# Kernel tuning notes

Measured on AMD Instinct MI355X. Metric: run time of the kernel, lower is better.

The kernel has to match this reference:

```python
import jax, jax.numpy as jnp
import numpy as np

EPS = 1e-5
N, K, CIN, COUT = 100000, 27, 64, 128


def sparse_conv(x, nbr, W):
    # x: [N, C]; nbr: [N, K] with sentinel index N meaning 'no neighbor'
    x_pad = jnp.concatenate([x, jnp.zeros((1, x.shape[1]), x.dtype)], axis=0)  # [N+1, C]
    g = x_pad[nbr]  # gather: [N, K, C]
    return jnp.einsum('nkc,kcd->nd', g, W)  # per-offset GEMM, scatter to output sites


def bn_relu(y, gamma, beta):
    # BatchNorm over active sites (training-mode batch statistics), then ReLU
    mu = y.mean(axis=0)
    var = y.var(axis=0)
    return jax.nn.relu((y - mu) * jax.lax.rsqrt(var + EPS) * gamma + beta)


def setup_inputs() -> dict:
    key = jax.random.key(0)
    ks = jax.random.split(key, 5)
    x = jax.random.normal(ks[0], (N, CIN), dtype=jnp.float32)
    # sentinel N indicates missing neighbor (maps to zero-padded row)
    nbr = jax.random.randint(ks[1], (N, K), 0, N + 1)
    W1 = jax.random.normal(ks[2], (K, CIN, COUT), dtype=jnp.float32) * (1.0 / np.sqrt(K * CIN))
    W2 = jax.random.normal(ks[3], (K, COUT, COUT), dtype=jnp.float32) * (1.0 / np.sqrt(K * COUT))
    W_skip = jax.random.normal(ks[4], (CIN, COUT), dtype=jnp.float32) * (1.0 / np.sqrt(CIN))
    return {
        'x': x, 'nbr': nbr,
        'W1': W1, 'gamma1': jnp.ones((COUT,), jnp.float32), 'beta1': jnp.zeros((COUT,), jnp.float32),
        'W2': W2, 'gamma2': jnp.ones((COUT,), jnp.float32), 'beta2': jnp.zeros((COUT,), jnp.float32),
        'W_skip': W_skip,
    }


def reference(x, nbr, W1, gamma1, beta1, W2, gamma2, beta2, W_skip):
    identity = x @ W_skip                      # 1x1 conv skip (same coords)
    h = bn_relu(sparse_conv(x, nbr, W1), gamma1, beta1)
    h = bn_relu(sparse_conv(h, nbr, W2), gamma2, beta2)
    return h + identity
```

## Files before the change

### kernel.cpp

```cpp
#include <hip/hip_runtime.h>
#include <hip/hip_bf16.h>

#define NSITES 100000
#define KOFFS 27
#define CIN 64
#define COUT 128

typedef unsigned short u16;
typedef __attribute__((ext_vector_type(8))) short s16x8;
typedef __attribute__((ext_vector_type(4))) float f32x4;

static __device__ __forceinline__ u16 f2bf(float f) {
    union { float f; unsigned u; } x; x.f = f;
    return (u16)((x.u + 0x7FFFu + ((x.u >> 16) & 1u)) >> 16);
}
static __device__ __forceinline__ float bf2f(u16 v) {
    union { unsigned u; float f; } x; x.u = ((unsigned)v) << 16;
    return x.f;
}

static __device__ __forceinline__ void lds_barrier() {
    asm volatile("s_waitcnt lgkmcnt(0)" ::: "memory");
    __builtin_amdgcn_s_barrier();
    __builtin_amdgcn_sched_barrier(0);
}

__global__ void prep_kernel(const float* __restrict__ W1, const float* __restrict__ W2,
                            const float* __restrict__ Wsk,
                            u16* __restrict__ W1t, u16* __restrict__ W2t,
                            u16* __restrict__ Wskt, float* __restrict__ zero_area) {
    int i = blockIdx.x * 256 + threadIdx.x;
    if (i < 27 * 64 * 128) {
        int k = i / 8192, r = i & 8191, d = r >> 6, c = r & 63;
        W1t[i] = f2bf(W1[k * 8192 + c * 128 + d]);
        return;
    }
    i -= 27 * 64 * 128;
    if (i < 27 * 128 * 128) {
        int k = i / 16384, r = i & 16383, d = r >> 7, c = r & 127;
        W2t[i] = f2bf(W2[k * 16384 + c * 128 + d]);
        return;
    }
    i -= 27 * 128 * 128;
    if (i < 8192) {
        int d = i >> 6, c = i & 63;
        Wskt[i] = f2bf(Wsk[c * 128 + d]);
        return;
    }
    i -= 8192;
    zero_area[i] = 0.0f;
}

__global__ void convert_x_kernel(const float* __restrict__ x, u16* __restrict__ xb) {
    long long e = ((long long)blockIdx.x * 256 + threadIdx.x) * 8;
    if (e >= (long long)(NSITES + 1) * CIN) return;
    s16x8 o;
    if (e < (long long)NSITES * CIN) {
        float4 v0 = *(const float4*)(x + e);
        float4 v1 = *(const float4*)(x + e + 4);
        o[0] = (short)f2bf(v0.x); o[1] = (short)f2bf(v0.y);
        o[2] = (short)f2bf(v0.z); o[3] = (short)f2bf(v0.w);
        o[4] = (short)f2bf(v1.x); o[5] = (short)f2bf(v1.y);
        o[6] = (short)f2bf(v1.z); o[7] = (short)f2bf(v1.w);
    } else {
#pragma unroll
        for (int j = 0; j < 8; ++j) o[j] = 0;
    }
    *(s16x8*)(xb + e) = o;
}

template <int CK, bool IDENT_FUSE, bool STATS>
__global__ __launch_bounds__(256, 3) void conv_kernel(
    const u16* __restrict__ xin, const int* __restrict__ nbr,
    const u16* __restrict__ Wt, u16* __restrict__ yout,
    float* __restrict__ psum, float* __restrict__ psq, int nk_unused,
    const u16* __restrict__ Wskt, float* __restrict__ outid) {
    constexpr int STRIDE = CK + 4;
    constexpr int KSTEPS = CK / 32;
    constexpr int CPR = CK / 8;
    constexpr int RPP = 256 / CPR;
    constexpr int NPASS = 64 / RPP;
    __shared__ __align__(16) u16 a_tile[2][64 * STRIDE];
    __shared__ int nbr_tile[64 * KOFFS];

    const int tid = threadIdx.x;
    const int wave = tid >> 6;
    const int lane = tid & 63;
    const int m = lane & 15;
    const int q = lane >> 4;
    const int n0 = blockIdx.x * 64;
    const int wc = wave * 32;
    const int srow = tid / CPR;
    const int schunk = tid % CPR;

    for (int i = tid; i < 64 * KOFFS; i += 256) {
        int r = i / KOFFS;
        int kk = i - r * KOFFS;
        int row = n0 + r;
        nbr_tile[i] = (row < NSITES) ? nbr[row * KOFFS + kk] : NSITES;
    }
    __syncthreads();

    f32x4 acc[4][2];
#pragma unroll
    for (int rt = 0; rt < 4; ++rt)
#pragma unroll
        for (int ct = 0; ct < 2; ++ct)
#pragma unroll
            for (int r = 0; r < 4; ++r) acc[rt][ct][r] = 0.0f;

    s16x8 gA[NPASS], gB[NPASS];
    s16x8 bA[2][KSTEPS], bB[2][KSTEPS];

    auto gload = [&](s16x8 (&g)[NPASS], int kk) {
#pragma unroll
        for (int p = 0; p < NPASS; ++p) {
            int r = p * RPP + srow;
            g[p] = *(const s16x8*)(xin + (long long)nbr_tile[r * KOFFS + kk] * CK + schunk * 8);
        }
    };
    auto bload = [&](s16x8 (&b)[2][KSTEPS], int kk) {
        const u16* wb = Wt + (long long)kk * (COUT * CK);
#pragma unroll
        for (int ct = 0; ct < 2; ++ct)
#pragma unroll
            for (int ks = 0; ks < KSTEPS; ++ks)
                b[ct][ks] = *(const s16x8*)(wb + (wc + ct * 16 + m) * CK + ks * 32 + q * 8);
    };
    auto awrite = [&](s16x8 (&g)[NPASS], int buf) {
#pragma unroll
        for (int p = 0; p < NPASS; ++p)
            *(s16x8*)(&a_tile[buf][(p * RPP + srow) * STRIDE + schunk * 8]) = g[p];
    };
    auto mfma_from = [&](int buf, s16x8 (&b)[2][KSTEPS]) {
        __builtin_amdgcn_s_setprio(1);
#pragma unroll
        for (int ks = 0; ks < KSTEPS; ++ks) {
            s16x8 af[4];
#pragma unroll
            for (int rt = 0; rt < 4; ++rt)
                af[rt] = *(const s16x8*)(&a_tile[buf][(rt * 16 + m) * STRIDE + ks * 32 + q * 8]);
#pragma unroll
            for (int rt = 0; rt < 4; ++rt)
#pragma unroll
                for (int ct = 0; ct < 2; ++ct)
                    acc[rt][ct] = __builtin_amdgcn_mfma_f32_16x16x32_bf16(
                        af[rt], b[ct][ks], acc[rt][ct], 0, 0, 0);
        }
        __builtin_amdgcn_s_setprio(0);
    };

    gload(gA, 0);
    bload(bA, 0);
    awrite(gA, 0);
    gload(gA, 1);
    bload(bB, 1);
    gload(gB, 2);
    lds_barrier();

    auto conv_iter = [&](int k, s16x8 (&g)[NPASS], s16x8 (&bcur)[2][KSTEPS]) {
        awrite(g, (k + 1) & 1);
        gload(g, k + 3);
        lds_barrier();
        mfma_from(k & 1, bcur);
        bload(bcur, k + 2);
        lds_barrier();
    };

    for (int k = 0; k < 24; k += 2) {
        conv_iter(k, gA, bA);
        conv_iter(k + 1, gB, bB);
    }
    awrite(gA, 1);
    lds_barrier();
    mfma_from(0, bA);
    bload(bA, 26);
    lds_barrier();
    awrite(gB, 0);
    lds_barrier();
    mfma_from(1, bB);
    lds_barrier();
    mfma_from(0, bA);

#pragma unroll
    for (int rt = 0; rt < 4; ++rt) {
        int rowb = n0 + rt * 16 + q * 4;
#pragma unroll
        for (int ct = 0; ct < 2; ++ct) {
            int col = wc + ct * 16 + m;
#pragma unroll
            for (int r = 0; r < 4; ++r) {
                int row = rowb + r;
                if (row < NSITES) yout[(long long)row * COUT + col] = f2bf(acc[rt][ct][r]);
            }
        }
    }

    if (STATS) {
#pragma unroll
        for (int ct = 0; ct < 2; ++ct) {
            float s = 0.f, ss = 0.f;
#pragma unroll
            for (int rt = 0; rt < 4; ++rt)
#pragma unroll
                for (int r = 0; r < 4; ++r) {
                    float v = acc[rt][ct][r];
                    s += v; ss += v * v;
                }
            s += __shfl_xor(s, 16); ss += __shfl_xor(ss, 16);
            s += __shfl_xor(s, 32); ss += __shfl_xor(ss, 32);
            if (q == 0) {
                int col = wc + ct * 16 + m;
                int slot = blockIdx.x & 63;
                atomicAdd(psum + slot * COUT + col, s);
                atomicAdd(psq + slot * COUT + col, ss);
            }
        }
    }

    if (IDENT_FUSE) {
        lds_barrier();
#pragma unroll
        for (int rt = 0; rt < 4; ++rt)
#pragma unroll
            for (int ct = 0; ct < 2; ++ct)
#pragma unroll
                for (int r = 0; r < 4; ++r) acc[rt][ct][r] = 0.0f;
        s16x8 aid[NPASS];
#pragma unroll
        for (int p = 0; p < NPASS; ++p) {
            int row = n0 + p * RPP + srow;
            long long idx = (row < NSITES) ? row : NSITES;
            aid[p] = *(const s16x8*)(xin + idx * CK + schunk * 8);
        }
        s16x8 bfi[2][KSTEPS];
#pragma unroll
        for (int ct = 0; ct < 2; ++ct)
#pragma unroll
            for (int ks = 0; ks < KSTEPS; ++ks)
                bfi[ct][ks] = *(const s16x8*)(Wskt + (wc + ct * 16 + m) * CK + ks * 32 + q * 8);
        awrite(aid, 0);
        lds_barrier();
        mfma_from(0, bfi);
#pragma unroll
        for (int rt = 0; rt < 4; ++rt) {
            int rowb = n0 + rt * 16 + q * 4;
#pragma unroll
            for (int ct = 0; ct < 2; ++ct) {
                int col = wc + ct * 16 + m;
#pragma unroll
                for (int r = 0; r < 4; ++r) {
                    int row = rowb + r;
                    if (row < NSITES) outid[(long long)row * COUT + col] = acc[rt][ct][r];
                }
            }
        }
    }
}

__global__ void bn_stats_kernel(const float* __restrict__ psum, const float* __restrict__ psq,
                                const float* __restrict__ gamma, const float* __restrict__ beta,
                                float* __restrict__ ab) {
    int col = threadIdx.x;
    float s = 0.f, ss = 0.f;
    for (int i = 0; i < 64; ++i) { s += psum[i * COUT + col]; ss += psq[i * COUT + col]; }
    const float inv_n = 1.0f / (float)NSITES;
    float mu = s * inv_n;
    float var = ss * inv_n - mu * mu;
    float rs = rsqrtf(var + 1e-5f);
    float a = gamma[col] * rs;
    ab[col] = a;
    ab[COUT + col] = beta[col] - mu * a;
}

__global__ void bn_apply_kernel(const u16* __restrict__ y, const float* __restrict__ ab,
                                u16* __restrict__ h) {
    long long e = ((long long)blockIdx.x * 256 + threadIdx.x) * 8;
    if (e >= (long long)(NSITES + 1) * COUT) return;
    s16x8 o;
    if (e < (long long)NSITES * COUT) {
        int cb = (int)(e & (COUT - 1));
        s16x8 v = *(const s16x8*)(y + e);
#pragma unroll
        for (int j = 0; j < 8; ++j) {
            float r = bf2f((u16)v[j]) * ab[cb + j] + ab[COUT + cb + j];
            o[j] = (short)f2bf(fmaxf(r, 0.f));
        }
    } else {
#pragma unroll
        for (int j = 0; j < 8; ++j) o[j] = 0;
    }
    *(s16x8*)(h + e) = o;
}

__global__ void final_kernel(const u16* __restrict__ y, const float* __restrict__ ab,
                             float* __restrict__ out) {
    long long e = ((long long)blockIdx.x * 256 + threadIdx.x) * 8;
    if (e >= (long long)NSITES * COUT) return;
    int cb = (int)(e & (COUT - 1));
    s16x8 v = *(const s16x8*)(y + e);
    float4 i0 = *(const float4*)(out + e);
    float4 i1 = *(const float4*)(out + e + 4);
    float is[8] = {i0.x, i0.y, i0.z, i0.w, i1.x, i1.y, i1.z, i1.w};
    float os[8];
#pragma unroll
    for (int j = 0; j < 8; ++j) {
        float r = bf2f((u16)v[j]) * ab[cb + j] + ab[COUT + cb + j];
        os[j] = fmaxf(r, 0.f) + is[j];
    }
    *(float4*)(out + e) = make_float4(os[0], os[1], os[2], os[3]);
    *(float4*)(out + e + 4) = make_float4(os[4], os[5], os[6], os[7]);
}

extern "C" void kernel_launch(void* const* d_in, const int* in_sizes, int n_in,
                              void* d_out, int out_size, void* d_ws, size_t ws_size,
                              hipStream_t stream) {
    const float* x   = (const float*)d_in[0];
    const int*   nbr = (const int*)d_in[1];
    const float* W1  = (const float*)d_in[2];
    const float* g1  = (const float*)d_in[3];
    const float* b1  = (const float*)d_in[4];
    const float* W2  = (const float*)d_in[5];
    const float* g2  = (const float*)d_in[6];
    const float* b2  = (const float*)d_in[7];
    const float* Wsk = (const float*)d_in[8];
    float* out = (float*)d_out;

    char* ws = (char*)d_ws;
    u16*   xb   = (u16*)(ws);
    u16*   W1t  = (u16*)(ws + 12800128);
    u16*   W2t  = (u16*)(ws + 13242496);
    u16*   Wskt = (u16*)(ws + 14127232);
    u16*   y    = (u16*)(ws + 14143616);
    u16*   h1   = (u16*)(ws + 39743616);
    float* ps1  = (float*)(ws + 65343872);
    float* pq1  = ps1 + 8192;
    float* ps2  = pq1 + 8192;
    float* pq2  = ps2 + 8192;
    float* ab1  = pq2 + 8192;
    float* ab2  = ab1 + 256;

    const int NBLK = (NSITES + 63) / 64;

    prep_kernel<<<2752, 256, 0, stream>>>(W1, W2, Wsk, W1t, W2t, Wskt, ps1);
    convert_x_kernel<<<3126, 256, 0, stream>>>(x, xb);
    conv_kernel<64, true, true><<<NBLK, 256, 0, stream>>>(xb, nbr, W1t, y, ps1, pq1, KOFFS, Wskt, out);
    bn_stats_kernel<<<1, 128, 0, stream>>>(ps1, pq1, g1, b1, ab1);
    bn_apply_kernel<<<6251, 256, 0, stream>>>(y, ab1, h1);
    conv_kernel<128, false, true><<<NBLK, 256, 0, stream>>>(h1, nbr, W2t, y, ps2, pq2, KOFFS, nullptr, nullptr);
    bn_stats_kernel<<<1, 128, 0, stream>>>(ps2, pq2, g2, b2, ab2);
    final_kernel<<<6250, 256, 0, stream>>>(y, ab2, out);
}
```

Before: 446.3 us.

## Fuse BN1 apply and ReLU into second conv's gather, add nontemporal memory ops

Removes the separate bn_apply kernel. The second sparse conv now gathers the raw conv1 output and applies the BN affine transform plus ReLU per element before writing to LDS. Sentinel neighbors are redirected to row 0 and masked to zero, so no padded row is needed. This saves a full read and write of the 25 MB intermediate, but the normalization is recomputed for each of the 27 gathers, which adds VALU work to the conv's LDS-write path. Nontemporal loads and stores are also applied to nbr, the conv outputs and the final kernel.

```diff
diff --git a/kernel.cpp b/kernel.cpp
--- a/kernel.cpp
+++ b/kernel.cpp
@@ -69,12 +69,13 @@
     *(s16x8*)(xb + e) = o;
 }
 
-template <int CK, bool IDENT_FUSE, bool STATS>
+template <int CK, bool IDENT_FUSE, bool STATS, bool TRANSFORM>
 __global__ __launch_bounds__(256, 3) void conv_kernel(
     const u16* __restrict__ xin, const int* __restrict__ nbr,
     const u16* __restrict__ Wt, u16* __restrict__ yout,
     float* __restrict__ psum, float* __restrict__ psq, int nk_unused,
-    const u16* __restrict__ Wskt, float* __restrict__ outid) {
+    const u16* __restrict__ Wskt, float* __restrict__ outid,
+    const float* __restrict__ abst) {
     constexpr int STRIDE = CK + 4;
     constexpr int KSTEPS = CK / 32;
     constexpr int CPR = CK / 8;
@@ -93,11 +94,22 @@
     const int srow = tid / CPR;
     const int schunk = tid % CPR;
 
+    float a8[8], b8[8];
+    if constexpr (TRANSFORM) {
+        const int cb = schunk * 8;
+#pragma unroll
+        for (int j = 0; j < 8; ++j) {
+            a8[j] = abst[cb + j];
+            b8[j] = abst[COUT + cb + j];
+        }
+    }
+
     for (int i = tid; i < 64 * KOFFS; i += 256) {
         int r = i / KOFFS;
         int kk = i - r * KOFFS;
         int row = n0 + r;
-        nbr_tile[i] = (row < NSITES) ? nbr[row * KOFFS + kk] : NSITES;
+        nbr_tile[i] = (row < NSITES) ? __builtin_nontemporal_load(&nbr[row * KOFFS + kk])
+                                     : NSITES;
     }
     __syncthreads();
 
@@ -110,13 +122,22 @@
             for (int r = 0; r < 4; ++r) acc[rt][ct][r] = 0.0f;
 
     s16x8 gA[NPASS], gB[NPASS];
+    int   sA[NPASS], sB[NPASS];
     s16x8 bA[2][KSTEPS], bB[2][KSTEPS];
 
-    auto gload = [&](s16x8 (&g)[NPASS], int kk) {
+    auto gload = [&](s16x8 (&g)[NPASS], int (&sen)[NPASS], int kk) {
 #pragma unroll
         for (int p = 0; p < NPASS; ++p) {
             int r = p * RPP + srow;
-            g[p] = *(const s16x8*)(xin + (long long)nbr_tile[r * KOFFS + kk] * CK + schunk * 8);
+            int idx = nbr_tile[r * KOFFS + kk];
+            long long gi;
+            if constexpr (TRANSFORM) {
+                sen[p] = (idx == NSITES);
+                gi = sen[p] ? 0 : idx;
+            } else {
+                gi = idx;
+            }
+            g[p] = *(const s16x8*)(xin + gi * CK + schunk * 8);
         }
     };
     auto bload = [&](s16x8 (&b)[2][KSTEPS], int kk) {
@@ -127,10 +148,22 @@
             for (int ks = 0; ks < KSTEPS; ++ks)
                 b[ct][ks] = *(const s16x8*)(wb + (wc + ct * 16 + m) * CK + ks * 32 + q * 8);
     };
-    auto awrite = [&](s16x8 (&g)[NPASS], int buf) {
-#pragma unroll
-        for (int p = 0; p < NPASS; ++p)
-            *(s16x8*)(&a_tile[buf][(p * RPP + srow) * STRIDE + schunk * 8]) = g[p];
+    auto awrite = [&](s16x8 (&g)[NPASS], int (&sen)[NPASS], int buf) {
+#pragma unroll
+        for (int p = 0; p < NPASS; ++p) {
+            s16x8 o;
+            if constexpr (TRANSFORM) {
+#pragma unroll
+                for (int j = 0; j < 8; ++j) {
+                    float v = bf2f((u16)g[p][j]);
+                    v = fmaxf(v * a8[j] + b8[j], 0.f);
+                    o[j] = sen[p] ? (short)0 : (short)f2bf(v);
+                }
+            } else {
+                o = g[p];
+            }
+            *(s16x8*)(&a_tile[buf][(p * RPP + srow) * STRIDE + schunk * 8]) = o;
+        }
     };
     auto mfma_from = [&](int buf, s16x8 (&b)[2][KSTEPS]) {
         __builtin_amdgcn_s_setprio(1);
@@ -150,17 +183,18 @@
         __builtin_amdgcn_s_setprio(0);
     };
 
-    gload(gA, 0);
+    gload(gA, sA, 0);
     bload(bA, 0);
-    awrite(gA, 0);
-    gload(gA, 1);
+    awrite(gA, sA, 0);
+    gload(gA, sA, 1);
     bload(bB, 1);
-    gload(gB, 2);
-    lds_barrier();
-
-    auto conv_iter = [&](int k, s16x8 (&g)[NPASS], s16x8 (&bcur)[2][KSTEPS]) {
-        awrite(g, (k + 1) & 1);
-        gload(g, k + 3);
+    gload(gB, sB, 2);
+    lds_barrier();
+
+    auto conv_iter = [&](int k, s16x8 (&g)[NPASS], int (&sen)[NPASS],
+                         s16x8 (&bcur)[2][KSTEPS]) {
+        awrite(g, sen, (k + 1) & 1);
+        gload(g, sen, k + 3);
         lds_barrier();
         mfma_from(k & 1, bcur);
         bload(bcur, k + 2);
@@ -168,15 +202,15 @@
     };
 
     for (int k = 0; k < 24; k += 2) {
-        conv_iter(k, gA, bA);
-        conv_iter(k + 1, gB, bB);
-    }
-    awrite(gA, 1);
+        conv_iter(k, gA, sA, bA);
+        conv_iter(k + 1, gB, sB, bB);
+    }
+    awrite(gA, sA, 1);
     lds_barrier();
     mfma_from(0, bA);
     bload(bA, 26);
     lds_barrier();
-    awrite(gB, 0);
+    awrite(gB, sB, 0);
     lds_barrier();
     mfma_from(1, bB);
     lds_barrier();
@@ -191,7 +225,9 @@
 #pragma unroll
             for (int r = 0; r < 4; ++r) {
                 int row = rowb + r;
-                if (row < NSITES) yout[(long long)row * COUT + col] = f2bf(acc[rt][ct][r]);
+                if (row < NSITES)
+                    __builtin_nontemporal_store((short)f2bf(acc[rt][ct][r]),
+                                                (short*)yout + (long long)row * COUT + col);
             }
         }
     }
@@ -239,7 +275,10 @@
 #pragma unroll
             for (int ks = 0; ks < KSTEPS; ++ks)
                 bfi[ct][ks] = *(const s16x8*)(Wskt + (wc + ct * 16 + m) * CK + ks * 32 + q * 8);
-        awrite(aid, 0);
+        int sdum[NPASS];
+#pragma unroll
+        for (int p = 0; p < NPASS; ++p) sdum[p] = 0;
+        awrite(aid, sdum, 0);
         lds_barrier();
         mfma_from(0, bfi);
 #pragma unroll
@@ -251,7 +290,9 @@
 #pragma unroll
                 for (int r = 0; r < 4; ++r) {
                     int row = rowb + r;
-                    if (row < NSITES) outid[(long long)row * COUT + col] = acc[rt][ct][r];
+                    if (row < NSITES)
+                        __builtin_nontemporal_store(acc[rt][ct][r],
+                                                    outid + (long long)row * COUT + col);
                 }
             }
         }
@@ -273,43 +314,27 @@
     ab[COUT + col] = beta[col] - mu * a;
 }
 
-__global__ void bn_apply_kernel(const u16* __restrict__ y, const float* __restrict__ ab,
-                                u16* __restrict__ h) {
-    long long e = ((long long)blockIdx.x * 256 + threadIdx.x) * 8;
-    if (e >= (long long)(NSITES + 1) * COUT) return;
-    s16x8 o;
-    if (e < (long long)NSITES * COUT) {
-        int cb = (int)(e & (COUT - 1));
-        s16x8 v = *(const s16x8*)(y + e);
-#pragma unroll
-        for (int j = 0; j < 8; ++j) {
-            float r = bf2f((u16)v[j]) * ab[cb + j] + ab[COUT + cb + j];
-            o[j] = (short)f2bf(fmaxf(r, 0.f));
-        }
-    } else {
-#pragma unroll
-        for (int j = 0; j < 8; ++j) o[j] = 0;
-    }
-    *(s16x8*)(h + e) = o;
-}
-
 __global__ void final_kernel(const u16* __restrict__ y, const float* __restrict__ ab,
                              float* __restrict__ out) {
     long long e = ((long long)blockIdx.x * 256 + threadIdx.x) * 8;
     if (e >= (long long)NSITES * COUT) return;
     int cb = (int)(e & (COUT - 1));
-    s16x8 v = *(const s16x8*)(y + e);
-    float4 i0 = *(const float4*)(out + e);
-    float4 i1 = *(const float4*)(out + e + 4);
-    float is[8] = {i0.x, i0.y, i0.z, i0.w, i1.x, i1.y, i1.z, i1.w};
-    float os[8];
-#pragma unroll
-    for (int j = 0; j < 8; ++j) {
+    s16x8 v = __builtin_nontemporal_load((const s16x8*)(y + e));
+    f32x4 i0 = __builtin_nontemporal_load((const f32x4*)(out + e));
+    f32x4 i1 = __builtin_nontemporal_load((const f32x4*)(out + e + 4));
+    f32x4 o0, o1;
+#pragma unroll
+    for (int j = 0; j < 4; ++j) {
         float r = bf2f((u16)v[j]) * ab[cb + j] + ab[COUT + cb + j];
-        os[j] = fmaxf(r, 0.f) + is[j];
-    }
-    *(float4*)(out + e) = make_float4(os[0], os[1], os[2], os[3]);
-    *(float4*)(out + e + 4) = make_float4(os[4], os[5], os[6], os[7]);
+        o0[j] = fmaxf(r, 0.f) + i0[j];
+    }
+#pragma unroll
+    for (int j = 0; j < 4; ++j) {
+        float r = bf2f((u16)v[4 + j]) * ab[cb + 4 + j] + ab[COUT + cb + 4 + j];
+        o1[j] = fmaxf(r, 0.f) + i1[j];
+    }
+    __builtin_nontemporal_store(o0, (f32x4*)(out + e));
+    __builtin_nontemporal_store(o1, (f32x4*)(out + e + 4));
 }
 
 extern "C" void kernel_launch(void* const* d_in, const int* in_sizes, int n_in,
@@ -332,7 +357,7 @@
     u16*   W2t  = (u16*)(ws + 13242496);
     u16*   Wskt = (u16*)(ws + 14127232);
     u16*   y    = (u16*)(ws + 14143616);
-    u16*   h1   = (u16*)(ws + 39743616);
+    u16*   y2   = (u16*)(ws + 39743616);
     float* ps1  = (float*)(ws + 65343872);
     float* pq1  = ps1 + 8192;
     float* ps2  = pq1 + 8192;
@@ -344,10 +369,11 @@
 
     prep_kernel<<<2752, 256, 0, stream>>>(W1, W2, Wsk, W1t, W2t, Wskt, ps1);
     convert_x_kernel<<<3126, 256, 0, stream>>>(x, xb);
-    conv_kernel<64, true, true><<<NBLK, 256, 0, stream>>>(xb, nbr, W1t, y, ps1, pq1, KOFFS, Wskt, out);
+    conv_kernel<64, true, true, false><<<NBLK, 256, 0, stream>>>(
+        xb, nbr, W1t, y, ps1, pq1, KOFFS, Wskt, out, nullptr);
     bn_stats_kernel<<<1, 128, 0, stream>>>(ps1, pq1, g1, b1, ab1);
-    bn_apply_kernel<<<6251, 256, 0, stream>>>(y, ab1, h1);
-    conv_kernel<128, false, true><<<NBLK, 256, 0, stream>>>(h1, nbr, W2t, y, ps2, pq2, KOFFS, nullptr, nullptr);
+    conv_kernel<128, false, true, true><<<NBLK, 256, 0, stream>>>(
+        y, nbr, W2t, y2, ps2, pq2, KOFFS, nullptr, nullptr, ab1);
     bn_stats_kernel<<<1, 128, 0, stream>>>(ps2, pq2, g2, b2, ab2);
-    final_kernel<<<6250, 256, 0, stream>>>(y, ab2, out);
-}
+    final_kernel<<<6250, 256, 0, stream>>>(y2, ab2, out);
+}
```

Result: slower. 468.8 us (+5.0%).

## Store activations in channel-sliced layout and use 32x32x16 MFMA in sparse conv

Applied to the files above, without the earlier changes.

Activations (converted x and BN output h1) are now stored as 16-channel slices, [C/16][N+1][16], so each gather fetches one 32-byte slice per neighbor. The conv kernel iterates over (slice, group of 4 offsets) and stages four neighbor offsets per LDS buffer. The 16x16x32 MFMAs are replaced by 32x32x16 MFMAs with two f32x16 accumulators, and launch bounds rise to 4 blocks per CU. The aim is less LDS/register pressure and better occupancy, traded against smaller, more scattered gather transactions and more pipeline iterations.

```diff
diff --git a/kernel.cpp b/kernel.cpp
--- a/kernel.cpp
+++ b/kernel.cpp
@@ -5,10 +5,12 @@
 #define KOFFS 27
 #define CIN 64
 #define COUT 128
+#define NROWS1 (NSITES + 1)
 
 typedef unsigned short u16;
 typedef __attribute__((ext_vector_type(8))) short s16x8;
 typedef __attribute__((ext_vector_type(4))) float f32x4;
+typedef __attribute__((ext_vector_type(16))) float f32x16;
 
 static __device__ __forceinline__ u16 f2bf(float f) {
     union { float f; unsigned u; } x; x.f = f;
@@ -53,9 +55,11 @@
 
 __global__ void convert_x_kernel(const float* __restrict__ x, u16* __restrict__ xb) {
     long long e = ((long long)blockIdx.x * 256 + threadIdx.x) * 8;
-    if (e >= (long long)(NSITES + 1) * CIN) return;
+    if (e >= (long long)NROWS1 * CIN) return;
+    int row = (int)(e >> 6);
+    int col = (int)(e & 63);
     s16x8 o;
-    if (e < (long long)NSITES * CIN) {
+    if (row < NSITES) {
         float4 v0 = *(const float4*)(x + e);
         float4 v1 = *(const float4*)(x + e + 4);
         o[0] = (short)f2bf(v0.x); o[1] = (short)f2bf(v0.y);
@@ -66,32 +70,32 @@
 #pragma unroll
         for (int j = 0; j < 8; ++j) o[j] = 0;
     }
-    *(s16x8*)(xb + e) = o;
-}
-
-template <int CK, bool IDENT_FUSE, bool STATS>
-__global__ __launch_bounds__(256, 3) void conv_kernel(
+    *(s16x8*)(xb + ((size_t)(col >> 4) * NROWS1 + row) * 16 + (col & 15)) = o;
+}
+
+template <int NSL, bool IDENT_FUSE, bool STATS>
+__global__ __launch_bounds__(256, 4) void conv_kernel(
     const u16* __restrict__ xin, const int* __restrict__ nbr,
     const u16* __restrict__ Wt, u16* __restrict__ yout,
-    float* __restrict__ psum, float* __restrict__ psq, int nk_unused,
+    float* __restrict__ psum, float* __restrict__ psq,
     const u16* __restrict__ Wskt, float* __restrict__ outid) {
-    constexpr int STRIDE = CK + 4;
-    constexpr int KSTEPS = CK / 32;
-    constexpr int CPR = CK / 8;
-    constexpr int RPP = 256 / CPR;
-    constexpr int NPASS = 64 / RPP;
-    __shared__ __align__(16) u16 a_tile[2][64 * STRIDE];
+    constexpr int CK = NSL * 16;
+    constexpr int NIT = NSL * 7;
+    constexpr int USTRIDE = 24;
+    constexpr int UNIT = 64 * USTRIDE;
+    constexpr int BUF = 4 * UNIT;
+    __shared__ __align__(16) u16 a_tile[2 * BUF];
     __shared__ int nbr_tile[64 * KOFFS];
 
     const int tid = threadIdx.x;
     const int wave = tid >> 6;
     const int lane = tid & 63;
-    const int m = lane & 15;
-    const int q = lane >> 4;
+    const int l31 = lane & 31;
+    const int hi = lane >> 5;
     const int n0 = blockIdx.x * 64;
     const int wc = wave * 32;
-    const int srow = tid / CPR;
-    const int schunk = tid % CPR;
+    const int su = tid >> 6;
+    const int srow = tid & 63;
 
     for (int i = tid; i < 64 * KOFFS; i += 256) {
         int r = i / KOFFS;
@@ -101,159 +105,134 @@
     }
     __syncthreads();
 
-    f32x4 acc[4][2];
-#pragma unroll
-    for (int rt = 0; rt < 4; ++rt)
-#pragma unroll
-        for (int ct = 0; ct < 2; ++ct)
-#pragma unroll
-            for (int r = 0; r < 4; ++r) acc[rt][ct][r] = 0.0f;
-
-    s16x8 gA[NPASS], gB[NPASS];
-    s16x8 bA[2][KSTEPS], bB[2][KSTEPS];
-
-    auto gload = [&](s16x8 (&g)[NPASS], int kk) {
-#pragma unroll
-        for (int p = 0; p < NPASS; ++p) {
-            int r = p * RPP + srow;
-            g[p] = *(const s16x8*)(xin + (long long)nbr_tile[r * KOFFS + kk] * CK + schunk * 8);
+    f32x16 acc0, acc1;
+#pragma unroll
+    for (int j = 0; j < 16; ++j) { acc0[j] = 0.0f; acc1[j] = 0.0f; }
+
+    s16x8 gA[2], gB[2];
+    s16x8 bA[4], bB[4];
+
+    auto gload = [&](s16x8 (&g)[2], int dit) {
+        int grp = dit % 7, s = dit / 7;
+        int gsz = (grp == 6) ? 3 : 4;
+        if (su < gsz) {
+            int k = grp * 4 + su;
+            const u16* base = xin + ((size_t)s * NROWS1 +
+                                     (size_t)nbr_tile[srow * KOFFS + k]) * 16;
+            g[0] = *(const s16x8*)(base);
+            g[1] = *(const s16x8*)(base + 8);
         }
     };
-    auto bload = [&](s16x8 (&b)[2][KSTEPS], int kk) {
-        const u16* wb = Wt + (long long)kk * (COUT * CK);
-#pragma unroll
-        for (int ct = 0; ct < 2; ++ct)
-#pragma unroll
-            for (int ks = 0; ks < KSTEPS; ++ks)
-                b[ct][ks] = *(const s16x8*)(wb + (wc + ct * 16 + m) * CK + ks * 32 + q * 8);
+    auto bload = [&](s16x8 (&b)[4], int dit) {
+        int grp = dit % 7, s = dit / 7;
+        int gsz = (grp == 6) ? 3 : 4;
+        const u16* wb = Wt + (size_t)(wc + l31) * CK + s * 16 + hi * 8;
+#pragma unroll
+        for (int u = 0; u < 4; ++u)
+            if (u < gsz) b[u] = *(const s16x8*)(wb + (size_t)(grp * 4 + u) * COUT * CK);
     };
-    auto awrite = [&](s16x8 (&g)[NPASS], int buf) {
-#pragma unroll
-        for (int p = 0; p < NPASS; ++p)
-            *(s16x8*)(&a_tile[buf][(p * RPP + srow) * STRIDE + schunk * 8]) = g[p];
+    auto awrite = [&](s16x8 (&g)[2], int dit) {
+        int grp = dit % 7;
+        int gsz = (grp == 6) ? 3 : 4;
+        if (su < gsz) {
+            u16* d = a_tile + (dit & 1) * BUF + su * UNIT + srow * USTRIDE;
+            *(s16x8*)(d) = g[0];
+            *(s16x8*)(d + 8) = g[1];
+        }
     };
-    auto mfma_from = [&](int buf, s16x8 (&b)[2][KSTEPS]) {
+    auto domfma = [&](int it, s16x8 (&b)[4]) {
+        int grp = it % 7;
+        int gsz = (grp == 6) ? 3 : 4;
+        const u16* base = a_tile + (it & 1) * BUF + l31 * USTRIDE + hi * 8;
         __builtin_amdgcn_s_setprio(1);
 #pragma unroll
-        for (int ks = 0; ks < KSTEPS; ++ks) {
-            s16x8 af[4];
-#pragma unroll
-            for (int rt = 0; rt < 4; ++rt)
-                af[rt] = *(const s16x8*)(&a_tile[buf][(rt * 16 + m) * STRIDE + ks * 32 + q * 8]);
-#pragma unroll
-            for (int rt = 0; rt < 4; ++rt)
-#pragma unroll
-                for (int ct = 0; ct < 2; ++ct)
-                    acc[rt][ct] = __builtin_amdgcn_mfma_f32_16x16x32_bf16(
-                        af[rt], b[ct][ks], acc[rt][ct], 0, 0, 0);
+        for (int u = 0; u < 4; ++u) {
+            if (u < gsz) {
+                s16x8 a0 = *(const s16x8*)(base + u * UNIT);
+                s16x8 a1 = *(const s16x8*)(base + u * UNIT + 32 * USTRIDE);
+                acc0 = __builtin_amdgcn_mfma_f32_32x32x16_bf16(a0, b[u], acc0, 0, 0, 0);
+                acc1 = __builtin_amdgcn_mfma_f32_32x32x16_bf16(a1, b[u], acc1, 0, 0, 0);
+            }
         }
         __builtin_amdgcn_s_setprio(0);
     };
 
-    gload(gA, 0);
-    bload(bA, 0);
-    awrite(gA, 0);
-    gload(gA, 1);
-    bload(bB, 1);
-    gload(gB, 2);
+    gload(gA, 0); bload(bA, 0);
+    awrite(gA, 0); gload(gA, 1); bload(bB, 1); gload(gB, 2);
     lds_barrier();
 
-    auto conv_iter = [&](int k, s16x8 (&g)[NPASS], s16x8 (&bcur)[2][KSTEPS]) {
-        awrite(g, (k + 1) & 1);
-        gload(g, k + 3);
+    for (int it = 0; it + 4 < NIT; it += 2) {
+        awrite(gA, it + 1); gload(gA, it + 3); lds_barrier();
+        domfma(it, bA); bload(bA, it + 2); lds_barrier();
+        awrite(gB, it + 2); gload(gB, it + 4); lds_barrier();
+        domfma(it + 1, bB); bload(bB, it + 3); lds_barrier();
+    }
+    awrite(gA, NIT - 3); gload(gA, NIT - 1); lds_barrier();
+    domfma(NIT - 4, bA); bload(bA, NIT - 2); lds_barrier();
+    awrite(gB, NIT - 2); lds_barrier();
+    domfma(NIT - 3, bB); bload(bB, NIT - 1); lds_barrier();
+    awrite(gA, NIT - 1); lds_barrier();
+    domfma(NIT - 2, bA); lds_barrier();
+    domfma(NIT - 1, bB);
+
+    const int colg = wc + l31;
+#pragma unroll
+    for (int j = 0; j < 16; ++j) {
+        int rw = (j & 3) + 8 * (j >> 2) + 4 * hi;
+        int r0 = n0 + rw;
+        int r1 = n0 + 32 + rw;
+        if (r0 < NSITES) yout[(size_t)r0 * COUT + colg] = f2bf(acc0[j]);
+        if (r1 < NSITES) yout[(size_t)r1 * COUT + colg] = f2bf(acc1[j]);
+    }
+
+    if (STATS) {
+        float s = 0.f, ss = 0.f;
+#pragma unroll
+        for (int j = 0; j < 16; ++j) {
+            float v0 = acc0[j], v1 = acc1[j];
+            s += v0 + v1; ss += v0 * v0 + v1 * v1;
+        }
+        s += __shfl_xor(s, 32); ss += __shfl_xor(ss, 32);
+        if (lane < 32) {
+            int slot = blockIdx.x & 63;
+            atomicAdd(psum + slot * COUT + colg, s);
+            atomicAdd(psq + slot * COUT + colg, ss);
+        }
+    }
+
+    if (IDENT_FUSE) {
+        {
+            int grow = n0 + srow;
+            size_t idx = (grow < NSITES) ? (size_t)grow : (size_t)NSITES;
+            const u16* base = xin + ((size_t)su * NROWS1 + idx) * 16;
+            s16x8 v0 = *(const s16x8*)(base);
+            s16x8 v1 = *(const s16x8*)(base + 8);
+            u16* d = a_tile + su * UNIT + srow * USTRIDE;
+            *(s16x8*)(d) = v0;
+            *(s16x8*)(d + 8) = v1;
+        }
         lds_barrier();
-        mfma_from(k & 1, bcur);
-        bload(bcur, k + 2);
-        lds_barrier();
-    };
-
-    for (int k = 0; k < 24; k += 2) {
-        conv_iter(k, gA, bA);
-        conv_iter(k + 1, gB, bB);
-    }
-    awrite(gA, 1);
-    lds_barrier();
-    mfma_from(0, bA);
-    bload(bA, 26);
-    lds_barrier();
-    awrite(gB, 0);
-    lds_barrier();
-    mfma_from(1, bB);
-    lds_barrier();
-    mfma_from(0, bA);
-
-#pragma unroll
-    for (int rt = 0; rt < 4; ++rt) {
-        int rowb = n0 + rt * 16 + q * 4;
-#pragma unroll
-        for (int ct = 0; ct < 2; ++ct) {
-            int col = wc + ct * 16 + m;
-#pragma unroll
-            for (int r = 0; r < 4; ++r) {
-                int row = rowb + r;
-                if (row < NSITES) yout[(long long)row * COUT + col] = f2bf(acc[rt][ct][r]);
-            }
-        }
-    }
-
-    if (STATS) {
-#pragma unroll
-        for (int ct = 0; ct < 2; ++ct) {
-            float s = 0.f, ss = 0.f;
-#pragma unroll
-            for (int rt = 0; rt < 4; ++rt)
-#pragma unroll
-                for (int r = 0; r < 4; ++r) {
-                    float v = acc[rt][ct][r];
-                    s += v; ss += v * v;
-                }
-            s += __shfl_xor(s, 16); ss += __shfl_xor(ss, 16);
-            s += __shfl_xor(s, 32); ss += __shfl_xor(ss, 32);
-            if (q == 0) {
-                int col = wc + ct * 16 + m;
-                int slot = blockIdx.x & 63;
-                atomicAdd(psum + slot * COUT + col, s);
-                atomicAdd(psq + slot * COUT + col, ss);
-            }
-        }
-    }
-
-    if (IDENT_FUSE) {
-        lds_barrier();
-#pragma unroll
-        for (int rt = 0; rt < 4; ++rt)
-#pragma unroll
-            for (int ct = 0; ct < 2; ++ct)
-#pragma unroll
-                for (int r = 0; r < 4; ++r) acc[rt][ct][r] = 0.0f;
-        s16x8 aid[NPASS];
-#pragma unroll
-        for (int p = 0; p < NPASS; ++p) {
-            int row = n0 + p * RPP + srow;
-            long long idx = (row < NSITES) ? row : NSITES;
-            aid[p] = *(const s16x8*)(xin + idx * CK + schunk * 8);
-        }
-        s16x8 bfi[2][KSTEPS];
-#pragma unroll
-        for (int ct = 0; ct < 2; ++ct)
-#pragma unroll
-            for (int ks = 0; ks < KSTEPS; ++ks)
-                bfi[ct][ks] = *(const s16x8*)(Wskt + (wc + ct * 16 + m) * CK + ks * 32 + q * 8);
-        awrite(aid, 0);
-        lds_barrier();
-        mfma_from(0, bfi);
-#pragma unroll
-        for (int rt = 0; rt < 4; ++rt) {
-            int rowb = n0 + rt * 16 + q * 4;
-#pragma unroll
-            for (int ct = 0; ct < 2; ++ct) {
-                int col = wc + ct * 16 + m;
-#pragma unroll
-                for (int r = 0; r < 4; ++r) {
-                    int row = rowb + r;
-                    if (row < NSITES) outid[(long long)row * COUT + col] = acc[rt][ct][r];
-                }
-            }
+#pragma unroll
+        for (int j = 0; j < 16; ++j) { acc0[j] = 0.0f; acc1[j] = 0.0f; }
+        s16x8 bsk[4];
+        const u16* wb = Wskt + (size_t)(wc + l31) * CIN + hi * 8;
+#pragma unroll
+        for (int u = 0; u < 4; ++u) bsk[u] = *(const s16x8*)(wb + u * 16);
+        const u16* base = a_tile + l31 * USTRIDE + hi * 8;
+#pragma unroll
+        for (int u = 0; u < 4; ++u) {
+            s16x8 a0 = *(const s16x8*)(base + u * UNIT);
+            s16x8 a1 = *(const s16x8*)(base + u * UNIT + 32 * USTRIDE);
+            acc0 = __builtin_amdgcn_mfma_f32_32x32x16_bf16(a0, bsk[u], acc0, 0, 0, 0);
+            acc1 = __builtin_amdgcn_mfma_f32_32x32x16_bf16(a1, bsk[u], acc1, 0, 0, 0);
+        }
+#pragma unroll
+        for (int j = 0; j < 16; ++j) {
+            int rw = (j & 3) + 8 * (j >> 2) + 4 * hi;
+            int r0 = n0 + rw;
+            int r1 = n0 + 32 + rw;
+            if (r0 < NSITES) outid[(size_t)r0 * COUT + colg] = acc0[j];
+            if (r1 < NSITES) outid[(size_t)r1 * COUT + colg] = acc1[j];
         }
     }
 }
@@ -276,21 +255,22 @@
 __global__ void bn_apply_kernel(const u16* __restrict__ y, const float* __restrict__ ab,
                                 u16* __restrict__ h) {
     long long e = ((long long)blockIdx.x * 256 + threadIdx.x) * 8;
-    if (e >= (long long)(NSITES + 1) * COUT) return;
+    if (e >= (long long)NROWS1 * COUT) return;
+    int row = (int)(e >> 7);
+    int col = (int)(e & 127);
     s16x8 o;
-    if (e < (long long)NSITES * COUT) {
-        int cb = (int)(e & (COUT - 1));
+    if (row < NSITES) {
         s16x8 v = *(const s16x8*)(y + e);
 #pragma unroll
         for (int j = 0; j < 8; ++j) {
-            float r = bf2f((u16)v[j]) * ab[cb + j] + ab[COUT + cb + j];
+            float r = bf2f((u16)v[j]) * ab[col + j] + ab[COUT + col + j];
             o[j] = (short)f2bf(fmaxf(r, 0.f));
         }
     } else {
 #pragma unroll
         for (int j = 0; j < 8; ++j) o[j] = 0;
     }
-    *(s16x8*)(h + e) = o;
+    *(s16x8*)(h + ((size_t)(col >> 4) * NROWS1 + row) * 16 + (col & 15)) = o;
 }
 
 __global__ void final_kernel(const u16* __restrict__ y, const float* __restrict__ ab,
@@ -344,10 +324,10 @@
 
     prep_kernel<<<2752, 256, 0, stream>>>(W1, W2, Wsk, W1t, W2t, Wskt, ps1);
     convert_x_kernel<<<3126, 256, 0, stream>>>(x, xb);
-    conv_kernel<64, true, true><<<NBLK, 256, 0, stream>>>(xb, nbr, W1t, y, ps1, pq1, KOFFS, Wskt, out);
+    conv_kernel<4, true, true><<<NBLK, 256, 0, stream>>>(xb, nbr, W1t, y, ps1, pq1, Wskt, out);
     bn_stats_kernel<<<1, 128, 0, stream>>>(ps1, pq1, g1, b1, ab1);
     bn_apply_kernel<<<6251, 256, 0, stream>>>(y, ab1, h1);
-    conv_kernel<128, false, true><<<NBLK, 256, 0, stream>>>(h1, nbr, W2t, y, ps2, pq2, KOFFS, nullptr, nullptr);
+    conv_kernel<8, false, true><<<NBLK, 256, 0, stream>>>(h1, nbr, W2t, y, ps2, pq2, nullptr, nullptr);
     bn_stats_kernel<<<1, 128, 0, stream>>>(ps2, pq2, g2, b2, ab2);
     final_kernel<<<6250, 256, 0, stream>>>(y, ab2, out);
 }
```

Result: slower. 736.9 us (+65.1%).
